# Optimization experiments

Hardware: AMD Instinct MI355X
Metric: run time of the kernel (lower is better)

Reference implementation:

```python
import jax, jax.numpy as jnp
import numpy as np

# --- static configuration (matches init_kwargs) ---
D = 16          # data_dim
H = 128         # hidden_dim
WID = 256       # vf_hidden_dim
LAB = 10        # label_dim
T = 200001      # len(ts) == len(intervals); logsig has T-1 rows
LSIG = 1 + D + D * (D - 1) // 2  # 137, depth-2 log-signature dim
NSTEPS = 100    # heun fixed-step: (ts[-1]-ts[0])/dt0 with dt0=0.01 over [0,1]
II, JJ = np.triu_indices(D, 1)   # depth-2 Hall pairs (i<j), row-major == HallSet order


def setup_inputs() -> dict:
    key = jax.random.key(0)
    ks = jax.random.split(key, 12)
    ts = jnp.linspace(0.0, 1.0, T, dtype=jnp.float32)
    logsig = jax.random.normal(ks[0], (T - 1, LSIG), jnp.float32) * 0.1
    x0 = jax.random.normal(ks[1], (D,), jnp.float32)

    def lin(kw, kb, fan_in, fan_out):
        bnd = 1.0 / np.sqrt(fan_in)
        w = jax.random.uniform(kw, (fan_in, fan_out), jnp.float32, -bnd, bnd)
        b = jax.random.uniform(kb, (fan_out,), jnp.float32, -bnd, bnd)
        return w, b

    l1_w, l1_b = lin(ks[2], ks[3], D, H)          # linear1: data_dim -> hidden
    w1, b1 = lin(ks[4], ks[5], H, WID)            # vf MLP layer 1
    w2, b2 = lin(ks[6], ks[7], WID, WID)          # vf MLP layer 2
    w3, b3 = lin(ks[8], ks[9], WID, D * H)        # vf MLP output layer
    l2_w, l2_b = lin(ks[10], ks[11], H, LAB)      # linear2: hidden -> label
    return dict(ts=ts, logsig=logsig, x0=x0, intervals=ts,
                l1_w=l1_w, l1_b=l1_b, w1=w1, b1=b1, w2=w2, b2=b2,
                w3=w3, b3=b3, l2_w=l2_w, l2_b=l2_b)


def reference(ts, logsig, x0, intervals, l1_w, l1_b, w1, b1, w2, b2, w3, b3, l2_w, l2_b):
    def mlp(y):  # VectorField: silu hidden layers, tanh final, scale=1
        h1 = jax.nn.silu(y @ w1 + b1)
        h2 = jax.nn.silu(h1 @ w2 + b2)
        return jnp.tanh(h2 @ w3 + b3)  # (D*H,)

    def field(t, y):
        # locate the log-signature interval containing t
        idx = jnp.clip(jnp.searchsorted(intervals[1:], t) + 1, 1, T - 1)
        ls = logsig[idx - 1]                       # (LSIG,)
        # primal + linearization of the vector field (forward-mode JVPs)
        vf_out, f_jvp = jax.linearize(mlp, y)
        W = vf_out.reshape(D, H)                   # vf directions, one per channel
        jvps = jax.vmap(f_jvp)(W).reshape(D, D, H) # jvps[k,i,:] = d vf_i / dy . W_k
        lie = jvps[II, JJ] - jvps[JJ, II]          # (D*(D-1)/2, H) Lie brackets
        res = ls[1:D + 1] @ W + ls[D + 1:] @ lie   # linear + bracket terms
        return res / (intervals[idx] - intervals[idx - 1])

    y0 = x0 @ l1_w + l1_b                          # linear1
    dt = (ts[-1] - ts[0]) / NSTEPS                 # fixed-step heun grid

    def step(carry, _):
        t, y = carry
        k1 = field(t, y)
        k2 = field(t + dt, y + dt * k1)
        return (t + dt, y + 0.5 * dt * (k1 + k2)), None

    (_, yT), _ = jax.lax.scan(step, (ts[0], y0), None, length=NSTEPS)
    return jax.nn.softmax(yT @ l2_w + l2_b, axis=-1)  # classification head
```

## Files before the change

kernel.cpp:

```cpp
#include <hip/hip_runtime.h>
#include <math.h>

#define AGENT __HIP_MEMORY_SCOPE_AGENT

constexpr int kNWG   = 32;
constexpr int kTPB   = 256;
constexpr int kD     = 16;
constexpr int kH     = 128;
constexpr int kW     = 256;
constexpr int kOut   = 2048;
constexpr int kLsig  = 137;
constexpr int kT     = 200001;
constexpr int kNRow  = 101;
constexpr int kNEval = 200;

constexpr int FLAGS_OFF = 0;
constexpr int IDX_OFF   = 32;
constexpr int INV_OFF   = 160;
constexpr int YB_OFF    = 288;
constexpr int H1B_OFF   = 416;
constexpr int H2B_OFF   = 672;
constexpr int WB_OFF    = 928;
constexpr int T1B_OFF   = 2976;
constexpr int T2B_OFF   = 7072;
constexpr int RSP_OFF   = 11168;

__device__ __forceinline__ float b2f(unsigned short u){
  union { unsigned int i; float f; } v; v.i = ((unsigned int)u) << 16; return v.f;
}
__device__ __forceinline__ unsigned short f2b(float f){
  unsigned int x = __float_as_uint(f);
  unsigned int r = x + 0x7fffu + ((x >> 16) & 1u);
  return (unsigned short)(r >> 16);
}
__device__ __forceinline__ float ldf(const void* p, size_t i, bool bf){
  return bf ? b2f(((const unsigned short*)p)[i]) : ((const float*)p)[i];
}
__device__ __forceinline__ float aload(const float* p){
  return __hip_atomic_load(p, __ATOMIC_RELAXED, AGENT);
}
__device__ __forceinline__ void astore(float* p, float v){
  __hip_atomic_store(p, v, __ATOMIC_RELAXED, AGENT);
}
__device__ __forceinline__ int pairidx(int i, int j){
  return i*15 - (i*(i-1))/2 + (j - i - 1);
}

__device__ __forceinline__ void gbar(unsigned* flags, int g, unsigned epoch, int tid){
  asm volatile("s_waitcnt vmcnt(0)" ::: "memory");
  __syncthreads();
  if (tid == 0)
    __hip_atomic_store(&flags[g], epoch, __ATOMIC_RELAXED, AGENT);
  if (tid < kNWG){
    int spins = 0;
    while (__hip_atomic_load(&flags[tid], __ATOMIC_RELAXED, AGENT) < epoch){
      __builtin_amdgcn_s_sleep(1);
      if (++spins > (1 << 16)) break;
    }
  }
  __syncthreads();
}

__global__ void cde_init(const void* __restrict__ tsp, const void* __restrict__ x0p,
                         const void* __restrict__ l1wp, const void* __restrict__ l1bp,
                         float* __restrict__ ws)
{
  const int tid = threadIdx.x;
  const bool bf = (((const unsigned*)tsp)[0] != 0u);
  const float ts0 = ldf(tsp, 0, bf);
  const float dt  = (ldf(tsp, kT-1, bf) - ts0) / 100.0f;

  if (tid < kNWG) ((unsigned*)(ws + FLAGS_OFF))[tid] = 0u;

  if (tid < kNRow){
    float t = ts0;
    for (int i = 0; i < tid; i++) t += dt;
    const int N1 = kT - 1;
    int lo = 0, hi = N1;
    while (lo < hi){
      int mid = (lo + hi) >> 1;
      if (ldf(tsp, 1 + mid, bf) < t) lo = mid + 1; else hi = mid;
    }
    int idx = lo + 1; if (idx > kT-1) idx = kT-1; if (idx < 1) idx = 1;
    ((int*)ws)[IDX_OFF + tid] = idx;
    float w = ldf(tsp, idx, bf) - ldf(tsp, idx-1, bf);
    ws[INV_OFF + tid] = (w > 0.f) ? (1.0f / w) : 0.f;
  }
  if (tid < kH){
    float acc = ldf(l1bp, tid, bf);
    for (int d2 = 0; d2 < kD; d2++) acc += ldf(x0p, d2, bf) * ldf(l1wp, d2*kH + tid, bf);
    ws[YB_OFF + tid] = acc;
  }
}

struct SMem {
  float w3T[64][257];
  float w1cT[8][129];
  float w2cT[8][257];
  float Wt[kD][129];
  float T1[kD][257];
  float h1[kW], h2[kW];
  float ls[kLsig + 7];
  float y[kH], ymid[kH], k1v[kH];
  float Urow[kW];
  float red[4][64];
  float tanhp[64];
  float s1p[8], s2p[8], b1c[8], b2c[8];
  float b3c[64];
  float Acol[kD];
  float lgts[16];
};
static_assert(sizeof(SMem) <= 120*1024, "LDS budget");

__global__ __launch_bounds__(kTPB, 1)
void cde_main(const void* __restrict__ tsp, const void* __restrict__ logsigp,
              const void* __restrict__ w1p, const void* __restrict__ b1p,
              const void* __restrict__ w2p, const void* __restrict__ b2p,
              const void* __restrict__ w3p, const void* __restrict__ b3p,
              const void* __restrict__ l2wp, const void* __restrict__ l2bp,
              float* __restrict__ ws, void* __restrict__ outp)
{
  __shared__ SMem s;
  const int g = blockIdx.x, tid = threadIdx.x;
  const int lane = tid & 63, wave = tid >> 6;
  const bool bf = (((const unsigned*)tsp)[0] != 0u);
  unsigned* flags = (unsigned*)(ws + FLAGS_OFF);
  float* h1b = ws + H1B_OFF;  float* h2b = ws + H2B_OFF;
  float* Wb  = ws + WB_OFF;   float* T1b = ws + T1B_OFF;
  float* T2b = ws + T2B_OFF;  float* rsp = ws + RSP_OFF;

  for (int i = tid; i < 8*kH; i += kTPB){ int o = i>>7, j = i&127; s.w1cT[o][j] = ldf(w1p, (size_t)j*kW + g*8 + o, bf); }
  for (int i = tid; i < 8*kW; i += kTPB){ int o = i>>8, n = i&255; s.w2cT[o][n] = ldf(w2p, (size_t)n*kW + g*8 + o, bf); }
  for (int i = tid; i < 64*kW; i += kTPB){ int n = i>>6, c = i&63;  s.w3T[c][n]  = ldf(w3p, (size_t)n*kOut + g*64 + c, bf); }
  if (tid < 8){ s.b1c[tid] = ldf(b1p, g*8 + tid, bf); s.b2c[tid] = ldf(b2p, g*8 + tid, bf); }
  if (tid < 64) s.b3c[tid] = ldf(b3p, g*64 + tid, bf);
  if (tid < kH) s.y[tid] = ws[YB_OFF + tid];
  const float dt  = (ldf(tsp, kT-1, bf) - ldf(tsp, 0, bf)) / 100.0f;
  const float dth = 0.5f * dt;
  __syncthreads();

  unsigned epoch = 0;

  for (int e = 0; e < kNEval; e++){
    const int r = (e + 1) >> 1;
    {
      const int idx = ((const int*)ws)[IDX_OFF + r];
      const float inv = ws[INV_OFF + r];
      for (int c = tid; c < kLsig; c += kTPB)
        s.ls[c] = ldf(logsigp, (size_t)(idx - 1)*kLsig + c, bf) * inv;
    }
    __syncthreads();
    const float* ycur = (e & 1) ? s.ymid : s.y;

    {
      const int o = tid >> 5, l = tid & 31;
      float acc = 0.f;
      #pragma unroll
      for (int jj = 0; jj < 4; jj++){ int j = jj*32 + l; acc += ycur[j] * s.w1cT[o][j]; }
      #pragma unroll
      for (int off = 16; off; off >>= 1) acc += __shfl_down(acc, off, 32);
      if (l == 0){
        float z = acc + s.b1c[o];
        float sg = 1.0f / (1.0f + expf(-z));
        s.s1p[o] = sg * (1.0f + z*(1.0f - sg));
        astore(h1b + g*8 + o, z * sg);
      }
    }
    gbar(flags, g, ++epoch, tid);
    s.h1[tid] = aload(h1b + tid);
    __syncthreads();

    {
      const int o = tid >> 5, l = tid & 31;
      float acc = 0.f;
      #pragma unroll
      for (int jj = 0; jj < 8; jj++){ int j = jj*32 + l; acc += s.h1[j] * s.w2cT[o][j]; }
      #pragma unroll
      for (int off = 16; off; off >>= 1) acc += __shfl_down(acc, off, 32);
      if (l == 0){
        float z = acc + s.b2c[o];
        float sg = 1.0f / (1.0f + expf(-z));
        s.s2p[o] = sg * (1.0f + z*(1.0f - sg));
        astore(h2b + g*8 + o, z * sg);
      }
    }
    gbar(flags, g, ++epoch, tid);
    s.h2[tid] = aload(h2b + tid);
    __syncthreads();

    {
      float acc = 0.f;
      #pragma unroll 8
      for (int j = 0; j < 64; j++) acc += s.h2[wave*64 + j] * s.w3T[lane][wave*64 + j];
      s.red[wave][lane] = acc;
    }
    __syncthreads();
    if (wave == 0){
      float z3 = s.red[0][lane] + s.red[1][lane] + s.red[2][lane] + s.red[3][lane] + s.b3c[lane];
      float Wv = tanhf(z3);
      s.tanhp[lane] = 1.0f - Wv*Wv;
      astore(Wb + g*64 + lane, Wv);
    }
    gbar(flags, g, ++epoch, tid);
    for (int i = tid; i < kD*kH; i += kTPB){ int k = i>>7, h = i&127; s.Wt[k][h] = aload(Wb + i); }
    __syncthreads();

    {
      const int outi = tid >> 1, half = tid & 1;
      const int k = outi >> 3, o = outi & 7;
      float acc = 0.f;
      #pragma unroll
      for (int jj = 0; jj < 64; jj++){ int j = jj*2 + half; acc += s.Wt[k][j] * s.w1cT[o][j]; }
      acc += __shfl_xor(acc, 1);
      if (half == 0) astore(T1b + k*kW + g*8 + o, acc * s.s1p[o]);
    }
    gbar(flags, g, ++epoch, tid);
    for (int i = tid; i < kD*kW; i += kTPB){ int k = i>>8, n = i&255; s.T1[k][n] = aload(T1b + i); }
    __syncthreads();

    {
      const int outi = tid >> 1, half = tid & 1;
      const int k = outi >> 3, o = outi & 7;
      float acc = 0.f;
      #pragma unroll 16
      for (int jj = 0; jj < 128; jj++){ int n = jj*2 + half; acc += s.T1[k][n] * s.w2cT[o][n]; }
      acc += __shfl_xor(acc, 1);
      if (half == 0) astore(T2b + k*kW + g*8 + o, acc * s.s2p[o]);
    }
    gbar(flags, g, ++epoch, tid);

    if (tid < kD){
      const int ig = g >> 1; const int k = tid; float v = 0.f;
      if (k < ig)      v =  s.ls[17 + pairidx(k, ig)];
      else if (k > ig) v = -s.ls[17 + pairidx(ig, k)];
      s.Acol[k] = v;
    }
    __syncthreads();
    {
      float u = 0.f; const int n = tid;
      #pragma unroll
      for (int k2 = 0; k2 < kD; k2++) u += s.Acol[k2] * aload(T2b + k2*kW + n);
      s.Urow[n] = u;
    }
    __syncthreads();
    {
      float acc = 0.f;
      #pragma unroll 8
      for (int j = 0; j < 64; j++) acc += s.Urow[wave*64 + j] * s.w3T[lane][wave*64 + j];
      s.red[wave][lane] = acc;
    }
    __syncthreads();
    if (wave == 0){
      float v = (s.red[0][lane] + s.red[1][lane] + s.red[2][lane] + s.red[3][lane]) * s.tanhp[lane];
      if (g < 2){
        float lin = 0.f; const int h = g*64 + lane;
        #pragma unroll
        for (int k2 = 0; k2 < kD; k2++) lin += s.ls[1 + k2] * s.Wt[k2][h];
        v += lin;
      }
      astore(rsp + g*64 + lane, v);
    }
    gbar(flags, g, ++epoch, tid);

    if (tid < kH){
      const int hh = tid >> 6, hl = tid & 63;
      float rs = 0.f;
      #pragma unroll
      for (int i2 = 0; i2 < kD; i2++) rs += aload(rsp + (2*i2 + hh)*64 + hl);
      if (!(e & 1)){ s.k1v[tid] = rs; s.ymid[tid] = s.y[tid] + dt * rs; }
      else         { s.y[tid] = s.y[tid] + dth * (s.k1v[tid] + rs); }
    }
    __syncthreads();
  }

  if (g == 0){
    if (tid < 10){
      float acc = ldf(l2bp, tid, bf);
      for (int h = 0; h < kH; h++) acc += s.y[h] * ldf(l2wp, (size_t)h*10 + tid, bf);
      s.lgts[tid] = acc;
    }
    __syncthreads();
    if (tid < 10){
      float m = s.lgts[0];
      #pragma unroll
      for (int i2 = 1; i2 < 10; i2++) m = fmaxf(m, s.lgts[i2]);
      float num = expf(s.lgts[tid] - m);
      float den = 0.f;
      #pragma unroll
      for (int i2 = 0; i2 < 10; i2++) den += expf(s.lgts[i2] - m);
      float v = num / den;
      if (bf) ((unsigned short*)outp)[tid] = f2b(v);
      else    ((float*)outp)[tid] = v;
    }
  }
}

extern "C" void kernel_launch(void* const* d_in, const int* in_sizes, int n_in,
                              void* d_out, int out_size, void* d_ws, size_t ws_size,
                              hipStream_t stream)
{
  const void* ts   = d_in[0];
  const void* lsig = d_in[1];
  const void* x0   = d_in[2];
  const void* l1w  = d_in[4];
  const void* l1b  = d_in[5];
  const void* w1   = d_in[6];
  const void* b1   = d_in[7];
  const void* w2   = d_in[8];
  const void* b2   = d_in[9];
  const void* w3   = d_in[10];
  const void* b3   = d_in[11];
  const void* l2w  = d_in[12];
  const void* l2b  = d_in[13];
  float* ws = (float*)d_ws;

  hipLaunchKernelGGL(cde_init, dim3(1), dim3(128), 0, stream, ts, x0, l1w, l1b, ws);
  hipLaunchKernelGGL(cde_main, dim3(kNWG), dim3(kTPB), 0, stream,
                     ts, lsig, w1, b1, w2, b2, w3, b3, l2w, l2b, ws, d_out);
}
```

Before: 4.801 ms.

## Compute MLP layers redundantly per block and replace grid barriers with tagged data flags

After: 9.098 ms. 89.5% more time.

```diff
diff --git a/kernel.cpp b/kernel.cpp
--- a/kernel.cpp
+++ b/kernel.cpp
@@ -13,17 +13,15 @@
 constexpr int kT     = 200001;
 constexpr int kNRow  = 101;
 constexpr int kNEval = 200;
-
-constexpr int FLAGS_OFF = 0;
-constexpr int IDX_OFF   = 32;
-constexpr int INV_OFF   = 160;
-constexpr int YB_OFF    = 288;
-constexpr int H1B_OFF   = 416;
-constexpr int H2B_OFF   = 672;
-constexpr int WB_OFF    = 928;
-constexpr int T1B_OFF   = 2976;
-constexpr int T2B_OFF   = 7072;
-constexpr int RSP_OFF   = 11168;
+constexpr int SPIN_MAX = 1 << 16;
+
+constexpr int FLAGS_OFF  = 0;
+constexpr int IDX_OFF    = 32;
+constexpr int INV_OFF    = 160;
+constexpr int YB_OFF     = 288;
+constexpr int T2B_OFF    = 416;
+constexpr int WTAG_U64   = 2256;
+constexpr int RSPTAG_U64 = 4304;
 
 __device__ __forceinline__ float b2f(unsigned short u){
   union { unsigned int i; float f; } v; v.i = ((unsigned int)u) << 16; return v.f;
@@ -36,11 +34,24 @@
 __device__ __forceinline__ float ldf(const void* p, size_t i, bool bf){
   return bf ? b2f(((const unsigned short*)p)[i]) : ((const float*)p)[i];
 }
+template<bool BF>
+__device__ __forceinline__ float ldT(const void* p, size_t i){
+  return BF ? b2f(((const unsigned short*)p)[i]) : ((const float*)p)[i];
+}
 __device__ __forceinline__ float aload(const float* p){
   return __hip_atomic_load(p, __ATOMIC_RELAXED, AGENT);
 }
 __device__ __forceinline__ void astore(float* p, float v){
   __hip_atomic_store(p, v, __ATOMIC_RELAXED, AGENT);
+}
+__device__ __forceinline__ unsigned long long aload64(const unsigned long long* p){
+  return __hip_atomic_load(p, __ATOMIC_RELAXED, AGENT);
+}
+__device__ __forceinline__ void astore64(unsigned long long* p, unsigned long long v){
+  __hip_atomic_store(p, v, __ATOMIC_RELAXED, AGENT);
+}
+__device__ __forceinline__ unsigned long long pk64(unsigned tag, float f){
+  return ((unsigned long long)tag << 32) | (unsigned long long)__float_as_uint(f);
 }
 __device__ __forceinline__ int pairidx(int i, int j){
   return i*15 - (i*(i-1))/2 + (j - i - 1);
@@ -55,7 +66,7 @@
     int spins = 0;
     while (__hip_atomic_load(&flags[tid], __ATOMIC_RELAXED, AGENT) < epoch){
       __builtin_amdgcn_s_sleep(1);
-      if (++spins > (1 << 16)) break;
+      if (++spins > SPIN_MAX) break;
     }
   }
   __syncthreads();
@@ -71,6 +82,10 @@
   const float dt  = (ldf(tsp, kT-1, bf) - ts0) / 100.0f;
 
   if (tid < kNWG) ((unsigned*)(ws + FLAGS_OFF))[tid] = 0u;
+  {
+    unsigned long long* tg = ((unsigned long long*)ws) + WTAG_U64;
+    for (int i = tid; i < 4096; i += kTPB) tg[i] = 0ULL;
+  }
 
   if (tid < kNRow){
     float t = ts0;
@@ -95,22 +110,215 @@
 
 struct SMem {
   float w3T[64][257];
-  float w1cT[8][129];
   float w2cT[8][257];
-  float Wt[kD][129];
+  alignas(16) float Wt[kD][kH];
   float T1[kD][257];
-  float h1[kW], h2[kW];
+  float h1[kW], s1p[kW];
+  float h2[kW], s2p[kW];
   float ls[kLsig + 7];
   float y[kH], ymid[kH], k1v[kH];
   float Urow[kW];
   float red[4][64];
   float tanhp[64];
-  float s1p[8], s2p[8], b1c[8], b2c[8];
+  float b1f[kW], b2f[kW];
   float b3c[64];
   float Acol[kD];
   float lgts[16];
 };
 static_assert(sizeof(SMem) <= 120*1024, "LDS budget");
+
+template<bool BF>
+__device__ void run_loop(SMem& s, const void* logsigp, const void* w1p, const void* w2p,
+                         float* ws, int g, int tid, int lane, int wave,
+                         float dt, float dth)
+{
+  unsigned* flags = (unsigned*)(ws + FLAGS_OFF);
+  float* T2b = ws + T2B_OFF;
+  unsigned long long* wtag   = ((unsigned long long*)ws) + WTAG_U64;
+  unsigned long long* rsptag = ((unsigned long long*)ws) + RSPTAG_U64;
+  unsigned epoch = 0;
+
+  for (int e = 0; e < kNEval; e++){
+    const unsigned tag = (unsigned)(e + 1);
+    const int r = (e + 1) >> 1;
+    {
+      const int idx = ((const int*)ws)[IDX_OFF + r];
+      const float inv = ws[INV_OFF + r];
+      for (int c = tid; c < kLsig; c += kTPB)
+        s.ls[c] = ldT<BF>(logsigp, (size_t)(idx - 1)*kLsig + c) * inv;
+    }
+    const float* ycur = (e & 1) ? s.ymid : s.y;
+
+    {
+      const int n = tid;
+      float p[32];
+      #pragma unroll
+      for (int l = 0; l < 32; l++){
+        float a = 0.f;
+        #pragma unroll
+        for (int jj = 0; jj < 4; jj++)
+          a += ycur[jj*32 + l] * ldT<BF>(w1p, (size_t)(jj*32 + l)*kW + n);
+        p[l] = a;
+      }
+      #pragma unroll
+      for (int off = 16; off >= 1; off >>= 1){
+        #pragma unroll
+        for (int l = 0; l < 16; l++)
+          if (l < off) p[l] += p[l + off];
+      }
+      float z = p[0] + s.b1f[n];
+      float sg = 1.0f / (1.0f + expf(-z));
+      s.h1[n]  = z * sg;
+      s.s1p[n] = sg * (1.0f + z*(1.0f - sg));
+    }
+    __syncthreads();
+
+    {
+      const int n = tid;
+      float p[32];
+      #pragma unroll
+      for (int l = 0; l < 32; l++){
+        float a = 0.f;
+        #pragma unroll
+        for (int jj = 0; jj < 8; jj++)
+          a += s.h1[jj*32 + l] * ldT<BF>(w2p, (size_t)(jj*32 + l)*kW + n);
+        p[l] = a;
+      }
+      #pragma unroll
+      for (int off = 16; off >= 1; off >>= 1){
+        #pragma unroll
+        for (int l = 0; l < 16; l++)
+          if (l < off) p[l] += p[l + off];
+      }
+      float z = p[0] + s.b2f[n];
+      float sg = 1.0f / (1.0f + expf(-z));
+      s.h2[n]  = z * sg;
+      s.s2p[n] = sg * (1.0f + z*(1.0f - sg));
+    }
+    __syncthreads();
+
+    {
+      float acc = 0.f;
+      #pragma unroll 8
+      for (int j = 0; j < 64; j++) acc += s.h2[wave*64 + j] * s.w3T[lane][wave*64 + j];
+      s.red[wave][lane] = acc;
+    }
+    __syncthreads();
+    if (wave == 0){
+      float z3 = s.red[0][lane] + s.red[1][lane] + s.red[2][lane] + s.red[3][lane] + s.b3c[lane];
+      float Wv = tanhf(z3);
+      s.tanhp[lane] = 1.0f - Wv*Wv;
+      astore64(wtag + g*64 + lane, pk64(tag, Wv));
+    }
+    {
+      unsigned long long v[8];
+      #pragma unroll
+      for (int j2 = 0; j2 < 8; j2++) v[j2] = aload64(wtag + tid + j2*kTPB);
+      #pragma unroll
+      for (int j2 = 0; j2 < 8; j2++){
+        int sp = 0;
+        while ((unsigned)(v[j2] >> 32) != tag){
+          __builtin_amdgcn_s_sleep(1);
+          v[j2] = aload64(wtag + tid + j2*kTPB);
+          if (++sp > SPIN_MAX) break;
+        }
+        int i = tid + j2*kTPB;
+        s.Wt[i>>7][i&127] = __uint_as_float((unsigned)v[j2]);
+      }
+    }
+    __syncthreads();
+
+    {
+      const int n = tid;
+      float ev[kD], ov[kD];
+      #pragma unroll
+      for (int k = 0; k < kD; k++){ ev[k] = 0.f; ov[k] = 0.f; }
+      const float s1 = s.s1p[n];
+      for (int j4 = 0; j4 < 32; j4++){
+        float a0 = ldT<BF>(w1p, (size_t)(4*j4+0)*kW + n);
+        float a1 = ldT<BF>(w1p, (size_t)(4*j4+1)*kW + n);
+        float a2 = ldT<BF>(w1p, (size_t)(4*j4+2)*kW + n);
+        float a3 = ldT<BF>(w1p, (size_t)(4*j4+3)*kW + n);
+        #pragma unroll
+        for (int k = 0; k < kD; k++){
+          float4 wt = *reinterpret_cast<const float4*>(&s.Wt[k][4*j4]);
+          ev[k] += wt.x * a0;
+          ov[k] += wt.y * a1;
+          ev[k] += wt.z * a2;
+          ov[k] += wt.w * a3;
+        }
+      }
+      #pragma unroll
+      for (int k = 0; k < kD; k++) s.T1[k][n] = (ev[k] + ov[k]) * s1;
+    }
+    __syncthreads();
+
+    {
+      const int outi = tid >> 1, half = tid & 1;
+      const int k = outi >> 3, o = outi & 7;
+      float acc = 0.f;
+      #pragma unroll 16
+      for (int jj = 0; jj < 128; jj++){ int n2 = jj*2 + half; acc += s.T1[k][n2] * s.w2cT[o][n2]; }
+      acc += __shfl_xor(acc, 1);
+      if (half == 0) astore(T2b + k*kW + g*8 + o, acc * s.s2p[g*8 + o]);
+    }
+    gbar(flags, g, ++epoch, tid);
+
+    if (tid < kD){
+      const int ig = g >> 1; const int k = tid; float v = 0.f;
+      if (k < ig)      v =  s.ls[17 + pairidx(k, ig)];
+      else if (k > ig) v = -s.ls[17 + pairidx(ig, k)];
+      s.Acol[k] = v;
+    }
+    __syncthreads();
+    {
+      float u = 0.f; const int n = tid;
+      #pragma unroll
+      for (int k2 = 0; k2 < kD; k2++) u += s.Acol[k2] * aload(T2b + k2*kW + n);
+      s.Urow[n] = u;
+    }
+    __syncthreads();
+    {
+      float acc = 0.f;
+      #pragma unroll 8
+      for (int j = 0; j < 64; j++) acc += s.Urow[wave*64 + j] * s.w3T[lane][wave*64 + j];
+      s.red[wave][lane] = acc;
+    }
+    __syncthreads();
+    if (wave == 0){
+      float v = (s.red[0][lane] + s.red[1][lane] + s.red[2][lane] + s.red[3][lane]) * s.tanhp[lane];
+      if (g < 2){
+        float lin = 0.f; const int h = g*64 + lane;
+        #pragma unroll
+        for (int k2 = 0; k2 < kD; k2++) lin += s.ls[1 + k2] * s.Wt[k2][h];
+        v += lin;
+      }
+      astore64(rsptag + g*64 + lane, pk64(tag, v));
+    }
+
+    if (tid < kH){
+      const int hh = tid >> 6, hl = tid & 63;
+      unsigned long long v[kD];
+      #pragma unroll
+      for (int i2 = 0; i2 < kD; i2++) v[i2] = aload64(rsptag + (2*i2 + hh)*64 + hl);
+      #pragma unroll
+      for (int i2 = 0; i2 < kD; i2++){
+        int sp = 0;
+        while ((unsigned)(v[i2] >> 32) != tag){
+          __builtin_amdgcn_s_sleep(1);
+          v[i2] = aload64(rsptag + (2*i2 + hh)*64 + hl);
+          if (++sp > SPIN_MAX) break;
+        }
+      }
+      float rs = 0.f;
+      #pragma unroll
+      for (int i2 = 0; i2 < kD; i2++) rs += __uint_as_float((unsigned)v[i2]);
+      if (!(e & 1)){ s.k1v[tid] = rs; s.ymid[tid] = s.y[tid] + dt * rs; }
+      else         { s.y[tid] = s.y[tid] + dth * (s.k1v[tid] + rs); }
+    }
+    __syncthreads();
+  }
+}
 
 __global__ __launch_bounds__(kTPB, 1)
 void cde_main(const void* __restrict__ tsp, const void* __restrict__ logsigp,
@@ -124,154 +332,19 @@
   const int g = blockIdx.x, tid = threadIdx.x;
   const int lane = tid & 63, wave = tid >> 6;
   const bool bf = (((const unsigned*)tsp)[0] != 0u);
-  unsigned* flags = (unsigned*)(ws + FLAGS_OFF);
-  float* h1b = ws + H1B_OFF;  float* h2b = ws + H2B_OFF;
-  float* Wb  = ws + WB_OFF;   float* T1b = ws + T1B_OFF;
-  float* T2b = ws + T2B_OFF;  float* rsp = ws + RSP_OFF;
-
-  for (int i = tid; i < 8*kH; i += kTPB){ int o = i>>7, j = i&127; s.w1cT[o][j] = ldf(w1p, (size_t)j*kW + g*8 + o, bf); }
+
   for (int i = tid; i < 8*kW; i += kTPB){ int o = i>>8, n = i&255; s.w2cT[o][n] = ldf(w2p, (size_t)n*kW + g*8 + o, bf); }
   for (int i = tid; i < 64*kW; i += kTPB){ int n = i>>6, c = i&63;  s.w3T[c][n]  = ldf(w3p, (size_t)n*kOut + g*64 + c, bf); }
-  if (tid < 8){ s.b1c[tid] = ldf(b1p, g*8 + tid, bf); s.b2c[tid] = ldf(b2p, g*8 + tid, bf); }
+  s.b1f[tid] = ldf(b1p, tid, bf);
+  s.b2f[tid] = ldf(b2p, tid, bf);
   if (tid < 64) s.b3c[tid] = ldf(b3p, g*64 + tid, bf);
   if (tid < kH) s.y[tid] = ws[YB_OFF + tid];
   const float dt  = (ldf(tsp, kT-1, bf) - ldf(tsp, 0, bf)) / 100.0f;
   const float dth = 0.5f * dt;
   __syncthreads();
 
-  unsigned epoch = 0;
-
-  for (int e = 0; e < kNEval; e++){
-    const int r = (e + 1) >> 1;
-    {
-      const int idx = ((const int*)ws)[IDX_OFF + r];
-      const float inv = ws[INV_OFF + r];
-      for (int c = tid; c < kLsig; c += kTPB)
-        s.ls[c] = ldf(logsigp, (size_t)(idx - 1)*kLsig + c, bf) * inv;
-    }
-    __syncthreads();
-    const float* ycur = (e & 1) ? s.ymid : s.y;
-
-    {
-      const int o = tid >> 5, l = tid & 31;
-      float acc = 0.f;
-      #pragma unroll
-      for (int jj = 0; jj < 4; jj++){ int j = jj*32 + l; acc += ycur[j] * s.w1cT[o][j]; }
-      #pragma unroll
-      for (int off = 16; off; off >>= 1) acc += __shfl_down(acc, off, 32);
-      if (l == 0){
-        float z = acc + s.b1c[o];
-        float sg = 1.0f / (1.0f + expf(-z));
-        s.s1p[o] = sg * (1.0f + z*(1.0f - sg));
-        astore(h1b + g*8 + o, z * sg);
-      }
-    }
-    gbar(flags, g, ++epoch, tid);
-    s.h1[tid] = aload(h1b + tid);
-    __syncthreads();
-
-    {
-      const int o = tid >> 5, l = tid & 31;
-      float acc = 0.f;
-      #pragma unroll
-      for (int jj = 0; jj < 8; jj++){ int j = jj*32 + l; acc += s.h1[j] * s.w2cT[o][j]; }
-      #pragma unroll
-      for (int off = 16; off; off >>= 1) acc += __shfl_down(acc, off, 32);
-      if (l == 0){
-        float z = acc + s.b2c[o];
-        float sg = 1.0f / (1.0f + expf(-z));
-        s.s2p[o] = sg * (1.0f + z*(1.0f - sg));
-        astore(h2b + g*8 + o, z * sg);
-      }
-    }
-    gbar(flags, g, ++epoch, tid);
-    s.h2[tid] = aload(h2b + tid);
-    __syncthreads();
-
-    {
-      float acc = 0.f;
-      #pragma unroll 8
-      for (int j = 0; j < 64; j++) acc += s.h2[wave*64 + j] * s.w3T[lane][wave*64 + j];
-      s.red[wave][lane] = acc;
-    }
-    __syncthreads();
-    if (wave == 0){
-      float z3 = s.red[0][lane] + s.red[1][lane] + s.red[2][lane] + s.red[3][lane] + s.b3c[lane];
-      float Wv = tanhf(z3);
-      s.tanhp[lane] = 1.0f - Wv*Wv;
-      astore(Wb + g*64 + lane, Wv);
-    }
-    gbar(flags, g, ++epoch, tid);
-    for (int i = tid; i < kD*kH; i += kTPB){ int k = i>>7, h = i&127; s.Wt[k][h] = aload(Wb + i); }
-    __syncthreads();
-
-    {
-      const int outi = tid >> 1, half = tid & 1;
-      const int k = outi >> 3, o = outi & 7;
-      float acc = 0.f;
-      #pragma unroll
-      for (int jj = 0; jj < 64; jj++){ int j = jj*2 + half; acc += s.Wt[k][j] * s.w1cT[o][j]; }
-      acc += __shfl_xor(acc, 1);
-      if (half == 0) astore(T1b + k*kW + g*8 + o, acc * s.s1p[o]);
-    }
-    gbar(flags, g, ++epoch, tid);
-    for (int i = tid; i < kD*kW; i += kTPB){ int k = i>>8, n = i&255; s.T1[k][n] = aload(T1b + i); }
-    __syncthreads();
-
-    {
-      const int outi = tid >> 1, half = tid & 1;
-      const int k = outi >> 3, o = outi & 7;
-      float acc = 0.f;
-      #pragma unroll 16
-      for (int jj = 0; jj < 128; jj++){ int n = jj*2 + half; acc += s.T1[k][n] * s.w2cT[o][n]; }
-      acc += __shfl_xor(acc, 1);
-      if (half == 0) astore(T2b + k*kW + g*8 + o, acc * s.s2p[o]);
-    }
-    gbar(flags, g, ++epoch, tid);
-
-    if (tid < kD){
-      const int ig = g >> 1; const int k = tid; float v = 0.f;
-      if (k < ig)      v =  s.ls[17 + pairidx(k, ig)];
-      else if (k > ig) v = -s.ls[17 + pairidx(ig, k)];
-      s.Acol[k] = v;
-    }
-    __syncthreads();
-    {
-      float u = 0.f; const int n = tid;
-      #pragma unroll
-      for (int k2 = 0; k2 < kD; k2++) u += s.Acol[k2] * aload(T2b + k2*kW + n);
-      s.Urow[n] = u;
-    }
-    __syncthreads();
-    {
-      float acc = 0.f;
-      #pragma unroll 8
-      for (int j = 0; j < 64; j++) acc += s.Urow[wave*64 + j] * s.w3T[lane][wave*64 + j];
-      s.red[wave][lane] = acc;
-    }
-    __syncthreads();
-    if (wave == 0){
-      float v = (s.red[0][lane] + s.red[1][lane] + s.red[2][lane] + s.red[3][lane]) * s.tanhp[lane];
-      if (g < 2){
-        float lin = 0.f; const int h = g*64 + lane;
-        #pragma unroll
-        for (int k2 = 0; k2 < kD; k2++) lin += s.ls[1 + k2] * s.Wt[k2][h];
-        v += lin;
-      }
-      astore(rsp + g*64 + lane, v);
-    }
-    gbar(flags, g, ++epoch, tid);
-
-    if (tid < kH){
-      const int hh = tid >> 6, hl = tid & 63;
-      float rs = 0.f;
-      #pragma unroll
-      for (int i2 = 0; i2 < kD; i2++) rs += aload(rsp + (2*i2 + hh)*64 + hl);
-      if (!(e & 1)){ s.k1v[tid] = rs; s.ymid[tid] = s.y[tid] + dt * rs; }
-      else         { s.y[tid] = s.y[tid] + dth * (s.k1v[tid] + rs); }
-    }
-    __syncthreads();
-  }
+  if (bf) run_loop<true >(s, logsigp, w1p, w2p, ws, g, tid, lane, wave, dt, dth);
+  else    run_loop<false>(s, logsigp, w1p, w2p, ws, g, tid, lane, wave, dt, dth);
 
   if (g == 0){
     if (tid < 10){
@@ -314,7 +387,7 @@
   const void* l2b  = d_in[13];
   float* ws = (float*)d_ws;
 
-  hipLaunchKernelGGL(cde_init, dim3(1), dim3(128), 0, stream, ts, x0, l1w, l1b, ws);
+  hipLaunchKernelGGL(cde_init, dim3(1), dim3(kTPB), 0, stream, ts, x0, l1w, l1b, ws);
   hipLaunchKernelGGL(cde_main, dim3(kNWG), dim3(kTPB), 0, stream,
                      ts, lsig, w1, b1, w2, b2, w3, b3, l2w, l2b, ws, d_out);
 }
```

## Replace two grid barriers with tagged 64-bit value/epoch flag exchange

Applied to the files above, without the earlier changes.

New measurement: 5.560 ms. 1.16x slower.

```diff
diff --git a/kernel.cpp b/kernel.cpp
--- a/kernel.cpp
+++ b/kernel.cpp
@@ -13,17 +13,16 @@
 constexpr int kT     = 200001;
 constexpr int kNRow  = 101;
 constexpr int kNEval = 200;
+constexpr int SPIN_MAX = 1 << 16;
 
 constexpr int FLAGS_OFF = 0;
 constexpr int IDX_OFF   = 32;
 constexpr int INV_OFF   = 160;
 constexpr int YB_OFF    = 288;
-constexpr int H1B_OFF   = 416;
-constexpr int H2B_OFF   = 672;
-constexpr int WB_OFF    = 928;
-constexpr int T1B_OFF   = 2976;
-constexpr int T2B_OFF   = 7072;
-constexpr int RSP_OFF   = 11168;
+constexpr int S_H1B = 416, S_H2B = 672, S_WB = 928, S_T1B = 2976, S_T2B = 7072, S_RSP = 11168;
+constexpr int F_H1B = 416, F_H2B = 672, F_T1B = 928, F_T2B = 5024;
+constexpr int F_WTAG = 4560, F_RSPTAG = 6608;
+constexpr size_t F_BYTES = 69248;
 
 __device__ __forceinline__ float b2f(unsigned short u){
   union { unsigned int i; float f; } v; v.i = ((unsigned int)u) << 16; return v.f;
@@ -41,6 +40,15 @@
 }
 __device__ __forceinline__ void astore(float* p, float v){
   __hip_atomic_store(p, v, __ATOMIC_RELAXED, AGENT);
+}
+__device__ __forceinline__ unsigned long long aload64(const unsigned long long* p){
+  return __hip_atomic_load(p, __ATOMIC_RELAXED, AGENT);
+}
+__device__ __forceinline__ void astore64(unsigned long long* p, unsigned long long v){
+  __hip_atomic_store(p, v, __ATOMIC_RELAXED, AGENT);
+}
+__device__ __forceinline__ unsigned long long pk64(unsigned tag, float f){
+  return ((unsigned long long)tag << 32) | (unsigned long long)__float_as_uint(f);
 }
 __device__ __forceinline__ int pairidx(int i, int j){
   return i*15 - (i*(i-1))/2 + (j - i - 1);
@@ -55,7 +63,7 @@
     int spins = 0;
     while (__hip_atomic_load(&flags[tid], __ATOMIC_RELAXED, AGENT) < epoch){
       __builtin_amdgcn_s_sleep(1);
-      if (++spins > (1 << 16)) break;
+      if (++spins > SPIN_MAX) break;
     }
   }
   __syncthreads();
@@ -63,7 +71,7 @@
 
 __global__ void cde_init(const void* __restrict__ tsp, const void* __restrict__ x0p,
                          const void* __restrict__ l1wp, const void* __restrict__ l1bp,
-                         float* __restrict__ ws)
+                         float* __restrict__ ws, int fast)
 {
   const int tid = threadIdx.x;
   const bool bf = (((const unsigned*)tsp)[0] != 0u);
@@ -71,6 +79,10 @@
   const float dt  = (ldf(tsp, kT-1, bf) - ts0) / 100.0f;
 
   if (tid < kNWG) ((unsigned*)(ws + FLAGS_OFF))[tid] = 0u;
+  if (fast){
+    unsigned long long* tg = ((unsigned long long*)ws) + F_WTAG;
+    for (int i = tid; i < 4096; i += 128) tg[i] = 0ULL;
+  }
 
   if (tid < kNRow){
     float t = ts0;
@@ -118,16 +130,21 @@
               const void* __restrict__ w2p, const void* __restrict__ b2p,
               const void* __restrict__ w3p, const void* __restrict__ b3p,
               const void* __restrict__ l2wp, const void* __restrict__ l2bp,
-              float* __restrict__ ws, void* __restrict__ outp)
+              float* __restrict__ ws, void* __restrict__ outp, int fast)
 {
   __shared__ SMem s;
   const int g = blockIdx.x, tid = threadIdx.x;
   const int lane = tid & 63, wave = tid >> 6;
   const bool bf = (((const unsigned*)tsp)[0] != 0u);
   unsigned* flags = (unsigned*)(ws + FLAGS_OFF);
-  float* h1b = ws + H1B_OFF;  float* h2b = ws + H2B_OFF;
-  float* Wb  = ws + WB_OFF;   float* T1b = ws + T1B_OFF;
-  float* T2b = ws + T2B_OFF;  float* rsp = ws + RSP_OFF;
+  float* h1b = ws + (fast ? F_H1B : S_H1B);
+  float* h2b = ws + (fast ? F_H2B : S_H2B);
+  float* T1b = ws + (fast ? F_T1B : S_T1B);
+  float* T2b = ws + (fast ? F_T2B : S_T2B);
+  float* Wb  = ws + S_WB;
+  float* rsp = ws + S_RSP;
+  unsigned long long* wtag   = ((unsigned long long*)ws) + F_WTAG;
+  unsigned long long* rsptag = ((unsigned long long*)ws) + F_RSPTAG;
 
   for (int i = tid; i < 8*kH; i += kTPB){ int o = i>>7, j = i&127; s.w1cT[o][j] = ldf(w1p, (size_t)j*kW + g*8 + o, bf); }
   for (int i = tid; i < 8*kW; i += kTPB){ int o = i>>8, n = i&255; s.w2cT[o][n] = ldf(w2p, (size_t)n*kW + g*8 + o, bf); }
@@ -142,6 +159,7 @@
   unsigned epoch = 0;
 
   for (int e = 0; e < kNEval; e++){
+    const unsigned tag = (unsigned)(e + 1);
     const int r = (e + 1) >> 1;
     {
       const int idx = ((const int*)ws)[IDX_OFF + r];
@@ -199,10 +217,28 @@
       float z3 = s.red[0][lane] + s.red[1][lane] + s.red[2][lane] + s.red[3][lane] + s.b3c[lane];
       float Wv = tanhf(z3);
       s.tanhp[lane] = 1.0f - Wv*Wv;
-      astore(Wb + g*64 + lane, Wv);
-    }
-    gbar(flags, g, ++epoch, tid);
-    for (int i = tid; i < kD*kH; i += kTPB){ int k = i>>7, h = i&127; s.Wt[k][h] = aload(Wb + i); }
+      if (fast) astore64(wtag + g*64 + lane, pk64(tag, Wv));
+      else      astore(Wb + g*64 + lane, Wv);
+    }
+    if (fast){
+      unsigned long long pv[8];
+      #pragma unroll
+      for (int j2 = 0; j2 < 8; j2++) pv[j2] = aload64(wtag + tid + j2*kTPB);
+      #pragma unroll
+      for (int j2 = 0; j2 < 8; j2++){
+        int sp = 0;
+        while ((unsigned)(pv[j2] >> 32) != tag){
+          __builtin_amdgcn_s_sleep(1);
+          pv[j2] = aload64(wtag + tid + j2*kTPB);
+          if (++sp > SPIN_MAX) break;
+        }
+        int i = tid + j2*kTPB;
+        s.Wt[i>>7][i&127] = __uint_as_float((unsigned)pv[j2]);
+      }
+    } else {
+      gbar(flags, g, ++epoch, tid);
+      for (int i = tid; i < kD*kH; i += kTPB){ int k = i>>7, h = i&127; s.Wt[k][h] = aload(Wb + i); }
+    }
     __syncthreads();
 
     {
@@ -258,15 +294,33 @@
         for (int k2 = 0; k2 < kD; k2++) lin += s.ls[1 + k2] * s.Wt[k2][h];
         v += lin;
       }
-      astore(rsp + g*64 + lane, v);
-    }
-    gbar(flags, g, ++epoch, tid);
+      if (fast) astore64(rsptag + g*64 + lane, pk64(tag, v));
+      else      astore(rsp + g*64 + lane, v);
+    }
+    if (!fast) gbar(flags, g, ++epoch, tid);
 
     if (tid < kH){
       const int hh = tid >> 6, hl = tid & 63;
       float rs = 0.f;
-      #pragma unroll
-      for (int i2 = 0; i2 < kD; i2++) rs += aload(rsp + (2*i2 + hh)*64 + hl);
+      if (fast){
+        unsigned long long pv[kD];
+        #pragma unroll
+        for (int i2 = 0; i2 < kD; i2++) pv[i2] = aload64(rsptag + (2*i2 + hh)*64 + hl);
+        #pragma unroll
+        for (int i2 = 0; i2 < kD; i2++){
+          int sp = 0;
+          while ((unsigned)(pv[i2] >> 32) != tag){
+            __builtin_amdgcn_s_sleep(1);
+            pv[i2] = aload64(rsptag + (2*i2 + hh)*64 + hl);
+            if (++sp > SPIN_MAX) break;
+          }
+        }
+        #pragma unroll
+        for (int i2 = 0; i2 < kD; i2++) rs += __uint_as_float((unsigned)pv[i2]);
+      } else {
+        #pragma unroll
+        for (int i2 = 0; i2 < kD; i2++) rs += aload(rsp + (2*i2 + hh)*64 + hl);
+      }
       if (!(e & 1)){ s.k1v[tid] = rs; s.ymid[tid] = s.y[tid] + dt * rs; }
       else         { s.y[tid] = s.y[tid] + dth * (s.k1v[tid] + rs); }
     }
@@ -313,8 +367,9 @@
   const void* l2w  = d_in[12];
   const void* l2b  = d_in[13];
   float* ws = (float*)d_ws;
-
-  hipLaunchKernelGGL(cde_init, dim3(1), dim3(128), 0, stream, ts, x0, l1w, l1b, ws);
+  const int fast = (ws_size >= F_BYTES) ? 1 : 0;
+
+  hipLaunchKernelGGL(cde_init, dim3(1), dim3(128), 0, stream, ts, x0, l1w, l1b, ws, fast);
   hipLaunchKernelGGL(cde_main, dim3(kNWG), dim3(kTPB), 0, stream,
-                     ts, lsig, w1, b1, w2, b2, w3, b3, l2w, l2b, ws, d_out);
-}
+                     ts, lsig, w1, b1, w2, b2, w3, b3, l2w, l2b, ws, d_out, fast);
+}
```

## Compute MLP layers 1-2 redundantly per block to drop two grid barriers

Applied to the files above, without the earlier changes.

Result: slower. 7.126 ms (+48.4%).

```diff
diff --git a/kernel.cpp b/kernel.cpp
--- a/kernel.cpp
+++ b/kernel.cpp
@@ -13,13 +13,12 @@
 constexpr int kT     = 200001;
 constexpr int kNRow  = 101;
 constexpr int kNEval = 200;
+constexpr int SPIN_MAX = 1 << 16;
 
 constexpr int FLAGS_OFF = 0;
 constexpr int IDX_OFF   = 32;
 constexpr int INV_OFF   = 160;
 constexpr int YB_OFF    = 288;
-constexpr int H1B_OFF   = 416;
-constexpr int H2B_OFF   = 672;
 constexpr int WB_OFF    = 928;
 constexpr int T1B_OFF   = 2976;
 constexpr int T2B_OFF   = 7072;
@@ -35,6 +34,10 @@
 }
 __device__ __forceinline__ float ldf(const void* p, size_t i, bool bf){
   return bf ? b2f(((const unsigned short*)p)[i]) : ((const float*)p)[i];
+}
+template<bool BF>
+__device__ __forceinline__ float ldT(const void* p, size_t i){
+  return BF ? b2f(((const unsigned short*)p)[i]) : ((const float*)p)[i];
 }
 __device__ __forceinline__ float aload(const float* p){
   return __hip_atomic_load(p, __ATOMIC_RELAXED, AGENT);
@@ -55,7 +58,7 @@
     int spins = 0;
     while (__hip_atomic_load(&flags[tid], __ATOMIC_RELAXED, AGENT) < epoch){
       __builtin_amdgcn_s_sleep(1);
-      if (++spins > (1 << 16)) break;
+      if (++spins > SPIN_MAX) break;
     }
   }
   __syncthreads();
@@ -99,18 +102,174 @@
   float w2cT[8][257];
   float Wt[kD][129];
   float T1[kD][257];
-  float h1[kW], h2[kW];
+  float h1[kW], s1p[kW];
+  float h2[kW], s2p[kW];
   float ls[kLsig + 7];
   float y[kH], ymid[kH], k1v[kH];
   float Urow[kW];
   float red[4][64];
   float tanhp[64];
-  float s1p[8], s2p[8], b1c[8], b2c[8];
+  float b1f[kW], b2f[kW];
   float b3c[64];
   float Acol[kD];
   float lgts[16];
 };
 static_assert(sizeof(SMem) <= 120*1024, "LDS budget");
+
+template<bool BF>
+__device__ void run_loop(SMem& s, const void* logsigp, const void* w1p, const void* w2p,
+                         float* ws, int g, int tid, int lane, int wave,
+                         float dt, float dth)
+{
+  unsigned* flags = (unsigned*)(ws + FLAGS_OFF);
+  float* Wb  = ws + WB_OFF;   float* T1b = ws + T1B_OFF;
+  float* T2b = ws + T2B_OFF;  float* rsp = ws + RSP_OFF;
+  unsigned epoch = 0;
+
+  for (int e = 0; e < kNEval; e++){
+    const int r = (e + 1) >> 1;
+    {
+      const int idx = ((const int*)ws)[IDX_OFF + r];
+      const float inv = ws[INV_OFF + r];
+      for (int c = tid; c < kLsig; c += kTPB)
+        s.ls[c] = ldT<BF>(logsigp, (size_t)(idx - 1)*kLsig + c) * inv;
+    }
+    __syncthreads();
+    const float* ycur = (e & 1) ? s.ymid : s.y;
+
+    {
+      const int n = tid;
+      float p[32];
+      #pragma unroll
+      for (int l = 0; l < 32; l++){
+        float a = 0.f;
+        #pragma unroll
+        for (int jj = 0; jj < 4; jj++)
+          a += ycur[jj*32 + l] * ldT<BF>(w1p, (size_t)(jj*32 + l)*kW + n);
+        p[l] = a;
+      }
+      #pragma unroll
+      for (int off = 16; off >= 1; off >>= 1){
+        #pragma unroll
+        for (int l = 0; l < 16; l++)
+          if (l < off) p[l] += p[l + off];
+      }
+      float z = p[0] + s.b1f[n];
+      float sg = 1.0f / (1.0f + expf(-z));
+      s.h1[n]  = z * sg;
+      s.s1p[n] = sg * (1.0f + z*(1.0f - sg));
+    }
+    __syncthreads();
+
+    {
+      const int n = tid;
+      float p[32];
+      #pragma unroll
+      for (int l = 0; l < 32; l++){
+        float a = 0.f;
+        #pragma unroll
+        for (int jj = 0; jj < 8; jj++)
+          a += s.h1[jj*32 + l] * ldT<BF>(w2p, (size_t)(jj*32 + l)*kW + n);
+        p[l] = a;
+      }
+      #pragma unroll
+      for (int off = 16; off >= 1; off >>= 1){
+        #pragma unroll
+        for (int l = 0; l < 16; l++)
+          if (l < off) p[l] += p[l + off];
+      }
+      float z = p[0] + s.b2f[n];
+      float sg = 1.0f / (1.0f + expf(-z));
+      s.h2[n]  = z * sg;
+      s.s2p[n] = sg * (1.0f + z*(1.0f - sg));
+    }
+    __syncthreads();
+
+    {
+      float acc = 0.f;
+      #pragma unroll 8
+      for (int j = 0; j < 64; j++) acc += s.h2[wave*64 + j] * s.w3T[lane][wave*64 + j];
+      s.red[wave][lane] = acc;
+    }
+    __syncthreads();
+    if (wave == 0){
+      float z3 = s.red[0][lane] + s.red[1][lane] + s.red[2][lane] + s.red[3][lane] + s.b3c[lane];
+      float Wv = tanhf(z3);
+      s.tanhp[lane] = 1.0f - Wv*Wv;
+      astore(Wb + g*64 + lane, Wv);
+    }
+    gbar(flags, g, ++epoch, tid);
+    for (int i = tid; i < kD*kH; i += kTPB){ int k = i>>7, h = i&127; s.Wt[k][h] = aload(Wb + i); }
+    __syncthreads();
+
+    {
+      const int outi = tid >> 1, half = tid & 1;
+      const int k = outi >> 3, o = outi & 7;
+      float acc = 0.f;
+      #pragma unroll
+      for (int jj = 0; jj < 64; jj++){ int j = jj*2 + half; acc += s.Wt[k][j] * s.w1cT[o][j]; }
+      acc += __shfl_xor(acc, 1);
+      if (half == 0) astore(T1b + k*kW + g*8 + o, acc * s.s1p[g*8 + o]);
+    }
+    gbar(flags, g, ++epoch, tid);
+    for (int i = tid; i < kD*kW; i += kTPB){ int k = i>>8, n = i&255; s.T1[k][n] = aload(T1b + i); }
+    __syncthreads();
+
+    {
+      const int outi = tid >> 1, half = tid & 1;
+      const int k = outi >> 3, o = outi & 7;
+      float acc = 0.f;
+      #pragma unroll 16
+      for (int jj = 0; jj < 128; jj++){ int n = jj*2 + half; acc += s.T1[k][n] * s.w2cT[o][n]; }
+      acc += __shfl_xor(acc, 1);
+      if (half == 0) astore(T2b + k*kW + g*8 + o, acc * s.s2p[g*8 + o]);
+    }
+    gbar(flags, g, ++epoch, tid);
+
+    if (tid < kD){
+      const int ig = g >> 1; const int k = tid; float v = 0.f;
+      if (k < ig)      v =  s.ls[17 + pairidx(k, ig)];
+      else if (k > ig) v = -s.ls[17 + pairidx(ig, k)];
+      s.Acol[k] = v;
+    }
+    __syncthreads();
+    {
+      float u = 0.f; const int n = tid;
+      #pragma unroll
+      for (int k2 = 0; k2 < kD; k2++) u += s.Acol[k2] * aload(T2b + k2*kW + n);
+      s.Urow[n] = u;
+    }
+    __syncthreads();
+    {
+      float acc = 0.f;
+      #pragma unroll 8
+      for (int j = 0; j < 64; j++) acc += s.Urow[wave*64 + j] * s.w3T[lane][wave*64 + j];
+      s.red[wave][lane] = acc;
+    }
+    __syncthreads();
+    if (wave == 0){
+      float v = (s.red[0][lane] + s.red[1][lane] + s.red[2][lane] + s.red[3][lane]) * s.tanhp[lane];
+      if (g < 2){
+        float lin = 0.f; const int h = g*64 + lane;
+        #pragma unroll
+        for (int k2 = 0; k2 < kD; k2++) lin += s.ls[1 + k2] * s.Wt[k2][h];
+        v += lin;
+      }
+      astore(rsp + g*64 + lane, v);
+    }
+    gbar(flags, g, ++epoch, tid);
+
+    if (tid < kH){
+      const int hh = tid >> 6, hl = tid & 63;
+      float rs = 0.f;
+      #pragma unroll
+      for (int i2 = 0; i2 < kD; i2++) rs += aload(rsp + (2*i2 + hh)*64 + hl);
+      if (!(e & 1)){ s.k1v[tid] = rs; s.ymid[tid] = s.y[tid] + dt * rs; }
+      else         { s.y[tid] = s.y[tid] + dth * (s.k1v[tid] + rs); }
+    }
+    __syncthreads();
+  }
+}
 
 __global__ __launch_bounds__(kTPB, 1)
 void cde_main(const void* __restrict__ tsp, const void* __restrict__ logsigp,
@@ -124,154 +283,20 @@
   const int g = blockIdx.x, tid = threadIdx.x;
   const int lane = tid & 63, wave = tid >> 6;
   const bool bf = (((const unsigned*)tsp)[0] != 0u);
-  unsigned* flags = (unsigned*)(ws + FLAGS_OFF);
-  float* h1b = ws + H1B_OFF;  float* h2b = ws + H2B_OFF;
-  float* Wb  = ws + WB_OFF;   float* T1b = ws + T1B_OFF;
-  float* T2b = ws + T2B_OFF;  float* rsp = ws + RSP_OFF;
 
   for (int i = tid; i < 8*kH; i += kTPB){ int o = i>>7, j = i&127; s.w1cT[o][j] = ldf(w1p, (size_t)j*kW + g*8 + o, bf); }
   for (int i = tid; i < 8*kW; i += kTPB){ int o = i>>8, n = i&255; s.w2cT[o][n] = ldf(w2p, (size_t)n*kW + g*8 + o, bf); }
   for (int i = tid; i < 64*kW; i += kTPB){ int n = i>>6, c = i&63;  s.w3T[c][n]  = ldf(w3p, (size_t)n*kOut + g*64 + c, bf); }
-  if (tid < 8){ s.b1c[tid] = ldf(b1p, g*8 + tid, bf); s.b2c[tid] = ldf(b2p, g*8 + tid, bf); }
+  s.b1f[tid] = ldf(b1p, tid, bf);
+  s.b2f[tid] = ldf(b2p, tid, bf);
   if (tid < 64) s.b3c[tid] = ldf(b3p, g*64 + tid, bf);
   if (tid < kH) s.y[tid] = ws[YB_OFF + tid];
   const float dt  = (ldf(tsp, kT-1, bf) - ldf(tsp, 0, bf)) / 100.0f;
   const float dth = 0.5f * dt;
   __syncthreads();
 
-  unsigned epoch = 0;
-
-  for (int e = 0; e < kNEval; e++){
-    const int r = (e + 1) >> 1;
-    {
-      const int idx = ((const int*)ws)[IDX_OFF + r];
-      const float inv = ws[INV_OFF + r];
-      for (int c = tid; c < kLsig; c += kTPB)
-        s.ls[c] = ldf(logsigp, (size_t)(idx - 1)*kLsig + c, bf) * inv;
-    }
-    __syncthreads();
-    const float* ycur = (e & 1) ? s.ymid : s.y;
-
-    {
-      const int o = tid >> 5, l = tid & 31;
-      float acc = 0.f;
-      #pragma unroll
-      for (int jj = 0; jj < 4; jj++){ int j = jj*32 + l; acc += ycur[j] * s.w1cT[o][j]; }
-      #pragma unroll
-      for (int off = 16; off; off >>= 1) acc += __shfl_down(acc, off, 32);
-      if (l == 0){
-        float z = acc + s.b1c[o];
-        float sg = 1.0f / (1.0f + expf(-z));
-        s.s1p[o] = sg * (1.0f + z*(1.0f - sg));
-        astore(h1b + g*8 + o, z * sg);
-      }
-    }
-    gbar(flags, g, ++epoch, tid);
-    s.h1[tid] = aload(h1b + tid);
-    __syncthreads();
-
-    {
-      const int o = tid >> 5, l = tid & 31;
-      float acc = 0.f;
-      #pragma unroll
-      for (int jj = 0; jj < 8; jj++){ int j = jj*32 + l; acc += s.h1[j] * s.w2cT[o][j]; }
-      #pragma unroll
-      for (int off = 16; off; off >>= 1) acc += __shfl_down(acc, off, 32);
-      if (l == 0){
-        float z = acc + s.b2c[o];
-        float sg = 1.0f / (1.0f + expf(-z));
-        s.s2p[o] = sg * (1.0f + z*(1.0f - sg));
-        astore(h2b + g*8 + o, z * sg);
-      }
-    }
-    gbar(flags, g, ++epoch, tid);
-    s.h2[tid] = aload(h2b + tid);
-    __syncthreads();
-
-    {
-      float acc = 0.f;
-      #pragma unroll 8
-      for (int j = 0; j < 64; j++) acc += s.h2[wave*64 + j] * s.w3T[lane][wave*64 + j];
-      s.red[wave][lane] = acc;
-    }
-    __syncthreads();
-    if (wave == 0){
-      float z3 = s.red[0][lane] + s.red[1][lane] + s.red[2][lane] + s.red[3][lane] + s.b3c[lane];
-      float Wv = tanhf(z3);
-      s.tanhp[lane] = 1.0f - Wv*Wv;
-      astore(Wb + g*64 + lane, Wv);
-    }
-    gbar(flags, g, ++epoch, tid);
-    for (int i = tid; i < kD*kH; i += kTPB){ int k = i>>7, h = i&127; s.Wt[k][h] = aload(Wb + i); }
-    __syncthreads();
-
-    {
-      const int outi = tid >> 1, half = tid & 1;
-      const int k = outi >> 3, o = outi & 7;
-      float acc = 0.f;
-      #pragma unroll
-      for (int jj = 0; jj < 64; jj++){ int j = jj*2 + half; acc += s.Wt[k][j] * s.w1cT[o][j]; }
-      acc += __shfl_xor(acc, 1);
-      if (half == 0) astore(T1b + k*kW + g*8 + o, acc * s.s1p[o]);
-    }
-    gbar(flags, g, ++epoch, tid);
-    for (int i = tid; i < kD*kW; i += kTPB){ int k = i>>8, n = i&255; s.T1[k][n] = aload(T1b + i); }
-    __syncthreads();
-
-    {
-      const int outi = tid >> 1, half = tid & 1;
-      const int k = outi >> 3, o = outi & 7;
-      float acc = 0.f;
-      #pragma unroll 16
-      for (int jj = 0; jj < 128; jj++){ int n = jj*2 + half; acc += s.T1[k][n] * s.w2cT[o][n]; }
-      acc += __shfl_xor(acc, 1);
-      if (half == 0) astore(T2b + k*kW + g*8 + o, acc * s.s2p[o]);
-    }
-    gbar(flags, g, ++epoch, tid);
-
-    if (tid < kD){
-      const int ig = g >> 1; const int k = tid; float v = 0.f;
-      if (k < ig)      v =  s.ls[17 + pairidx(k, ig)];
-      else if (k > ig) v = -s.ls[17 + pairidx(ig, k)];
-      s.Acol[k] = v;
-    }
-    __syncthreads();
-    {
-      float u = 0.f; const int n = tid;
-      #pragma unroll
-      for (int k2 = 0; k2 < kD; k2++) u += s.Acol[k2] * aload(T2b + k2*kW + n);
-      s.Urow[n] = u;
-    }
-    __syncthreads();
-    {
-      float acc = 0.f;
-      #pragma unroll 8
-      for (int j = 0; j < 64; j++) acc += s.Urow[wave*64 + j] * s.w3T[lane][wave*64 + j];
-      s.red[wave][lane] = acc;
-    }
-    __syncthreads();
-    if (wave == 0){
-      float v = (s.red[0][lane] + s.red[1][lane] + s.red[2][lane] + s.red[3][lane]) * s.tanhp[lane];
-      if (g < 2){
-        float lin = 0.f; const int h = g*64 + lane;
-        #pragma unroll
-        for (int k2 = 0; k2 < kD; k2++) lin += s.ls[1 + k2] * s.Wt[k2][h];
-        v += lin;
-      }
-      astore(rsp + g*64 + lane, v);
-    }
-    gbar(flags, g, ++epoch, tid);
-
-    if (tid < kH){
-      const int hh = tid >> 6, hl = tid & 63;
-      float rs = 0.f;
-      #pragma unroll
-      for (int i2 = 0; i2 < kD; i2++) rs += aload(rsp + (2*i2 + hh)*64 + hl);
-      if (!(e & 1)){ s.k1v[tid] = rs; s.ymid[tid] = s.y[tid] + dt * rs; }
-      else         { s.y[tid] = s.y[tid] + dth * (s.k1v[tid] + rs); }
-    }
-    __syncthreads();
-  }
+  if (bf) run_loop<true >(s, logsigp, w1p, w2p, ws, g, tid, lane, wave, dt, dth);
+  else    run_loop<false>(s, logsigp, w1p, w2p, ws, g, tid, lane, wave, dt, dth);
 
   if (g == 0){
     if (tid < 10){
```
